# Performance work log

Hardware: AMD Instinct MI355X
Metric: run time of the kernel (lower is better)

The kernel has to match this reference:

```python
import jax, jax.numpy as jnp
import numpy as np

B, N, M, G = 2, 8192, 8192, 256
X_MIN = Y_MIN = -35.0
CELL = abs(2.0 * X_MIN / G)  # cell size, as in construct_batched_cuda_grid


def setup_inputs() -> dict:
    key = jax.random.key(0)
    k1, k2, k3, k4, k5 = jax.random.split(key, 5)
    p_i = jax.random.uniform(k1, (B, N, 3), jnp.float32, -34.0, 34.0)
    p_j = jax.random.uniform(k2, (B, M, 3), jnp.float32, -34.0, 34.0)
    mos = jax.random.normal(k3, (B, 2, G, G), jnp.float32)
    error_p_i_flow = jax.random.uniform(k4, (B, N), jnp.float32)
    nearest_flow = jax.random.randint(k5, (B, N, 1), 0, M, jnp.int32)
    return {"p_i": p_i, "mos": mos, "p_j": p_j,
            "error_p_i_flow": error_p_i_flow, "nearest_flow": nearest_flow}


def _knn1_l1(x, y):
    # brute-force 1-NN with L1 (norm=1) distance, matching knn_points(..., K=1, norm=1)
    # build (B,N,M) dist one coordinate at a time to avoid a (B,N,M,3) intermediate
    d = (jnp.abs(x[:, :, None, 0] - y[:, None, :, 0])
         + jnp.abs(x[:, :, None, 1] - y[:, None, :, 1])
         + jnp.abs(x[:, :, None, 2] - y[:, None, :, 2]))
    return jnp.min(d, axis=-1), jnp.argmin(d, axis=-1)


def reference(p_i, mos, p_j, error_p_i_flow, nearest_flow):
    # NN_loss with reduction='none' -> error_p_i_rigid = (cham_x + cham_y)/2 (needs N==M)
    cham_x, nearest_rigid = _knn1_l1(p_i, p_j)  # (B,N), (B,N)
    cham_y, _ = _knn1_l1(p_j, p_i)              # (B,M)
    error_p_i_rigid = (cham_x + cham_y) * 0.5

    dynamic = error_p_i_flow > error_p_i_rigid             # (B,N) bool
    idx = jnp.where(dynamic, nearest_flow[..., 0], nearest_rigid)  # (B,N)
    art_labels = dynamic.astype(jnp.int32)                 # (B,N) in {0,1}

    # batched gather p_j[b, idx[b]]
    p_j_by_nn = jnp.take_along_axis(p_j, idx[..., None], axis=1)  # (B,N,3)

    # construct_batched_cuda_grid: scatter labels into (B,G,G), -1 elsewhere
    shift = jnp.array([X_MIN, Y_MIN], jnp.float32)
    cell_idx = ((p_j_by_nn[:, :, :2] - shift) / CELL).astype(jnp.int32)  # (B,N,2)
    bs = jnp.repeat(jnp.arange(B), N)
    grid = -jnp.ones((B, G, G), jnp.int32)
    grid = grid.at[bs,
                   cell_idx[..., 0].reshape(-1),
                   cell_idx[..., 1].reshape(-1)].set(art_labels.reshape(-1))

    # CrossEntropyLoss(ignore_index=-1), mean over non-ignored cells
    logp = jax.nn.log_softmax(mos, axis=1)                 # (B,C,G,G)
    valid = grid >= 0
    tgt = jnp.clip(grid, 0, None)
    lp = jnp.take_along_axis(logp, tgt[:, None], axis=1)[:, 0]  # (B,G,G)
    loss = -jnp.where(valid, lp, 0.0).sum() / jnp.maximum(valid.sum(), 1).astype(lp.dtype)
    return loss
```

## Files before the change

### kernel.cpp

```cpp
#include <hip/hip_runtime.h>
#include <float.h>

#define B_ 2
#define N_ 8192
#define G_ 256
constexpr float X_MIN_F = -35.0f;
constexpr float CELL_F  = 0.2734375f;

using u64 = unsigned long long;

#define OFF_ACCUM 524288
#define OFF_PX    524352

template<int CC>
__global__ __launch_bounds__(256) void nn_kernel(const float* __restrict__ p_i,
                                                 const float* __restrict__ p_j,
                                                 u64* __restrict__ px,
                                                 float* __restrict__ py,
                                                 int* __restrict__ grid,
                                                 unsigned* __restrict__ accum)
{
    constexpr int COLS = N_ / CC;
    constexpr int NB   = 32 * CC;
    const int dir  = blockIdx.z >> 1;
    const int b    = blockIdx.z & 1;
    const int tid  = threadIdx.x;
    const int row0 = blockIdx.x * 1024 + tid * 4;
    const int c0   = blockIdx.y * COLS;

    const float* __restrict__ P = dir ? p_j : p_i;
    const float* __restrict__ Q = dir ? p_i : p_j;

    __shared__ __align__(16) float q[COLS * 3];
    for (int t = tid; t < COLS * 3 / 4; t += 256)
        ((float4*)q)[t] = ((const float4*)(Q + ((size_t)b * N_ + c0) * 3))[t];

    {
        const int lin = blockIdx.x + 8 * (blockIdx.y + CC * blockIdx.z);
        constexpr int PER = 32768 / NB;
        if (tid < PER)
            ((uint4*)grid)[lin * PER + tid] = make_uint4(~0u, ~0u, ~0u, ~0u);
        if (lin == 0 && tid < 4) accum[tid] = 0u;
    }

    const float4* pp = (const float4*)(P + ((size_t)b * N_ + row0) * 3);
    float4 r0 = pp[0], r1 = pp[1], r2 = pp[2];
    float px_[4] = {r0.x, r0.w, r1.z, r2.y};
    float py_[4] = {r0.y, r1.x, r1.w, r2.z};
    float pz_[4] = {r0.z, r1.y, r2.x, r2.w};

    float best[4];
#pragma unroll
    for (int r = 0; r < 4; r++) best[r] = FLT_MAX;

    __syncthreads();

    if (dir == 0) {
        int gcol[4] = {0, 0, 0, 0};
        for (int jg = 0; jg < COLS; jg += 8) {
            const float4* qv = (const float4*)&q[jg * 3];
            float4 v0 = qv[0], v1 = qv[1], v2 = qv[2];
            float4 v3 = qv[3], v4 = qv[4], v5 = qv[5];
            float qx[8] = {v0.x, v0.w, v1.z, v2.y, v3.x, v3.w, v4.z, v5.y};
            float qy[8] = {v0.y, v1.x, v1.w, v2.z, v3.y, v4.x, v4.w, v5.z};
            float qz[8] = {v0.z, v1.y, v2.x, v2.w, v3.z, v4.y, v5.x, v5.w};
#pragma unroll
            for (int r = 0; r < 4; r++) {
                float d[8];
#pragma unroll
                for (int k = 0; k < 8; k++)
                    d[k] = (fabsf(px_[r] - qx[k]) + fabsf(py_[r] - qy[k]))
                           + fabsf(pz_[r] - qz[k]);
                float m01 = fminf(d[0], d[1]), m23 = fminf(d[2], d[3]);
                float m45 = fminf(d[4], d[5]), m67 = fminf(d[6], d[7]);
                float m = fminf(fminf(m01, m23), fminf(m45, m67));
                bool lt = m < best[r];
                best[r] = lt ? m : best[r];
                gcol[r] = lt ? jg : gcol[r];
            }
        }
        int bidx[4];
#pragma unroll
        for (int r = 0; r < 4; r++) {
            const float4* qv = (const float4*)&q[gcol[r] * 3];
            float4 v0 = qv[0], v1 = qv[1], v2 = qv[2];
            float4 v3 = qv[3], v4 = qv[4], v5 = qv[5];
            float qx[8] = {v0.x, v0.w, v1.z, v2.y, v3.x, v3.w, v4.z, v5.y};
            float qy[8] = {v0.y, v1.x, v1.w, v2.z, v3.y, v4.x, v4.w, v5.z};
            float qz[8] = {v0.z, v1.y, v2.x, v2.w, v3.z, v4.y, v5.x, v5.w};
            int kk = 0;
#pragma unroll
            for (int k = 7; k >= 0; k--) {
                float d = (fabsf(px_[r] - qx[k]) + fabsf(py_[r] - qy[k]))
                          + fabsf(pz_[r] - qz[k]);
                kk = (d == best[r]) ? k : kk;
            }
            bidx[r] = c0 + gcol[r] + kk;
        }
        const size_t o = (size_t)blockIdx.y * (B_ * N_) + b * N_ + row0;
#pragma unroll
        for (int r = 0; r < 4; r++)
            px[o + r] = ((u64)__float_as_uint(best[r]) << 32) | (unsigned)bidx[r];
    } else {
        for (int jg = 0; jg < COLS; jg += 8) {
            const float4* qv = (const float4*)&q[jg * 3];
            float4 v0 = qv[0], v1 = qv[1], v2 = qv[2];
            float4 v3 = qv[3], v4 = qv[4], v5 = qv[5];
            float qx[8] = {v0.x, v0.w, v1.z, v2.y, v3.x, v3.w, v4.z, v5.y};
            float qy[8] = {v0.y, v1.x, v1.w, v2.z, v3.y, v4.x, v4.w, v5.z};
            float qz[8] = {v0.z, v1.y, v2.x, v2.w, v3.z, v4.y, v5.x, v5.w};
#pragma unroll
            for (int r = 0; r < 4; r++) {
#pragma unroll
                for (int k = 0; k < 8; k++) {
                    float d = (fabsf(px_[r] - qx[k]) + fabsf(py_[r] - qy[k]))
                              + fabsf(pz_[r] - qz[k]);
                    best[r] = fminf(best[r], d);
                }
            }
        }
        const size_t o = (size_t)blockIdx.y * (B_ * N_) + b * N_ + row0;
#pragma unroll
        for (int r = 0; r < 4; r++) py[o + r] = best[r];
    }
}

template<int CC>
__global__ __launch_bounds__(256) void reduce_scatter_kernel(
    const u64* __restrict__ px, const float* __restrict__ py,
    const float* __restrict__ flow, const int* __restrict__ nflow,
    const float* __restrict__ Pj, int* __restrict__ grid)
{
    __shared__ u64      sbx[64];
    __shared__ unsigned sby[64];
    const int tid = threadIdx.x;
    const int p   = tid & 63;
    const int g   = tid >> 6;
    constexpr int CPG = CC / 4;

    if (tid < 64) { sbx[tid] = ~0ull; sby[tid] = ~0u; }
    __syncthreads();

    const int pt = blockIdx.x * 64 + p;
    u64   bx = ~0ull;
    float by = FLT_MAX;
#pragma unroll
    for (int k = 0; k < CPG; k++) {
        int c = g * CPG + k;
        u64 v = px[(size_t)c * (B_ * N_) + pt];
        bx = v < bx ? v : bx;
        by = fminf(by, py[(size_t)c * (B_ * N_) + pt]);
    }
    atomicMin(&sbx[p], bx);
    atomicMin(&sby[p], __float_as_uint(by));
    __syncthreads();

    if (tid < 64) {
        u64 fx = sbx[tid];
        float dx = __uint_as_float((unsigned)(fx >> 32));
        float dy = __uint_as_float(sby[tid]);
        float rigid = (dx + dy) * 0.5f;

        const int i = blockIdx.x * 64 + tid;
        const int b = i >> 13;
        const int n = i & (N_ - 1);

        bool dyn  = flow[i] > rigid;
        int label = dyn ? 1 : 0;
        int idx   = dyn ? nflow[i] : (int)(unsigned)(fx & 0xFFFFFFFFull);

        const float* qp = Pj + ((size_t)b * N_ + idx) * 3;
        float xx = qp[0], yy = qp[1];

        int cx = (int)((xx - X_MIN_F) / CELL_F);
        int cy = (int)((yy - X_MIN_F) / CELL_F);

        atomicMax(&grid[(b << 16) + cx * G_ + cy], (n << 1) | label);
    }
}

__global__ __launch_bounds__(256) void ce_kernel(const float* __restrict__ mos,
                                                 const int* __restrict__ grid,
                                                 float* __restrict__ accum,
                                                 float* __restrict__ out)
{
    int i = blockIdx.x * 256 + threadIdx.x;
    float lsum = 0.0f;
    int   lcnt = 0;

    int packed = grid[i];
    if (packed >= 0) {
        int b    = i >> 16;
        int cell = i & 0xFFFF;
        float m0 = mos[((size_t)b * 2 + 0) * 65536 + cell];
        float m1 = mos[((size_t)b * 2 + 1) * 65536 + cell];
        float mx = fmaxf(m0, m1);
        float lse = logf(expf(m0 - mx) + expf(m1 - mx));
        float sh  = ((packed & 1) ? m1 : m0) - mx;
        lsum = sh - lse;
        lcnt = 1;
    }

#pragma unroll
    for (int o = 32; o > 0; o >>= 1) {
        lsum += __shfl_down(lsum, o);
        lcnt += __shfl_down(lcnt, o);
    }
    __shared__ float wsum[4];
    __shared__ int   wcnt[4];
    int wave = threadIdx.x >> 6;
    if ((threadIdx.x & 63) == 0) { wsum[wave] = lsum; wcnt[wave] = lcnt; }
    __syncthreads();
    if (threadIdx.x == 0) {
        float s = wsum[0] + wsum[1] + wsum[2] + wsum[3];
        int   c = wcnt[0] + wcnt[1] + wcnt[2] + wcnt[3];
        atomicAdd(&accum[0], s);
        atomicAdd((int*)&accum[1], c);
        __threadfence();
        unsigned t = atomicAdd((unsigned*)&accum[2], 1u);
        if (t == gridDim.x - 1) {
            float S = atomicAdd(&accum[0], 0.0f);
            int   C = atomicAdd((int*)&accum[1], 0);
            out[0] = -S / (float)(C > 0 ? C : 1);
        }
    }
}

template<int CC>
static void run(const float* p_i, const float* mos, const float* p_j,
                const float* flow, const int* nflow, float* out,
                char* ws, hipStream_t stream)
{
    int*   grid  = (int*)ws;
    float* accum = (float*)(ws + OFF_ACCUM);
    u64*   px    = (u64*)(ws + OFF_PX);
    float* py    = (float*)(ws + OFF_PX + (size_t)CC * B_ * N_ * 8);

    dim3 g(8, CC, 4);
    nn_kernel<CC><<<g, 256, 0, stream>>>(p_i, p_j, px, py, (int*)grid,
                                         (unsigned*)accum);
    reduce_scatter_kernel<CC><<<256, 256, 0, stream>>>(px, py, flow, nflow,
                                                       p_j, grid);
    ce_kernel<<<(B_ * G_ * G_) / 256, 256, 0, stream>>>(mos, grid, accum, out);
}

extern "C" void kernel_launch(void* const* d_in, const int* in_sizes, int n_in,
                              void* d_out, int out_size, void* d_ws, size_t ws_size,
                              hipStream_t stream)
{
    const float* p_i   = (const float*)d_in[0];
    const float* mos   = (const float*)d_in[1];
    const float* p_j   = (const float*)d_in[2];
    const float* flow  = (const float*)d_in[3];
    const int*   nflow = (const int*)d_in[4];
    float* out = (float*)d_out;
    char* ws = (char*)d_ws;

    if (ws_size >= OFF_PX + (size_t)64 * B_ * N_ * 12)
        run<64>(p_i, mos, p_j, flow, nflow, out, ws, stream);
    else if (ws_size >= OFF_PX + (size_t)32 * B_ * N_ * 12)
        run<32>(p_i, mos, p_j, flow, nflow, out, ws, stream);
    else
        run<8>(p_i, mos, p_j, flow, nflow, out, ws, stream);
}
```

Measured before the change: 128.1 us.

## Fuse both NN directions into one pass using symmetric distance column minima

The L1 distance is symmetric, so the second nearest-neighbour direction (p_j to p_i) no longer launches its own set of blocks. Instead, the p_i-row pass also reduces each distance tile along columns, using permlane32_swap, a per-wave LDS scratch and xor shuffles. Per-block column partial minima go to the workspace, and the reduce kernel merges the 8 row-block partials. This removes about half of the distance arithmetic and halves the grid, at the cost of extra cross-lane reduction work and LDS traffic in every 8-column step. The main loop now reads the query points from global memory, which are uniform per block, instead of from LDS.

```diff
diff --git a/kernel.cpp b/kernel.cpp
--- a/kernel.cpp
+++ b/kernel.cpp
@@ -16,24 +16,27 @@
 __global__ __launch_bounds__(256) void nn_kernel(const float* __restrict__ p_i,
                                                  const float* __restrict__ p_j,
                                                  u64* __restrict__ px,
-                                                 float* __restrict__ py,
+                                                 float* __restrict__ colpart,
                                                  int* __restrict__ grid,
                                                  unsigned* __restrict__ accum)
 {
     constexpr int COLS = N_ / CC;
-    constexpr int NB   = 32 * CC;
-    const int dir  = blockIdx.z >> 1;
-    const int b    = blockIdx.z & 1;
+    constexpr int NB   = 16 * CC;
+    const int b    = blockIdx.z;
     const int tid  = threadIdx.x;
+    const int lane = tid & 63;
+    const int w    = tid >> 6;
     const int row0 = blockIdx.x * 1024 + tid * 4;
     const int c0   = blockIdx.y * COLS;
 
-    const float* __restrict__ P = dir ? p_j : p_i;
-    const float* __restrict__ Q = dir ? p_i : p_j;
-
     __shared__ __align__(16) float q[COLS * 3];
+    __shared__ float sc[4][8][35];
+    __shared__ float colW[4][COLS];
+
+    const float* __restrict__ Qg = p_j + ((size_t)b * N_ + c0) * 3;
+
     for (int t = tid; t < COLS * 3 / 4; t += 256)
-        ((float4*)q)[t] = ((const float4*)(Q + ((size_t)b * N_ + c0) * 3))[t];
+        ((float4*)q)[t] = ((const float4*)Qg)[t];
 
     {
         const int lin = blockIdx.x + 8 * (blockIdx.y + CC * blockIdx.z);
@@ -43,91 +46,98 @@
         if (lin == 0 && tid < 4) accum[tid] = 0u;
     }
 
-    const float4* pp = (const float4*)(P + ((size_t)b * N_ + row0) * 3);
+    const float4* pp = (const float4*)(p_i + ((size_t)b * N_ + row0) * 3);
     float4 r0 = pp[0], r1 = pp[1], r2 = pp[2];
     float px_[4] = {r0.x, r0.w, r1.z, r2.y};
     float py_[4] = {r0.y, r1.x, r1.w, r2.z};
     float pz_[4] = {r0.z, r1.y, r2.x, r2.w};
 
-    float best[4];
-#pragma unroll
-    for (int r = 0; r < 4; r++) best[r] = FLT_MAX;
-
-    __syncthreads();
-
-    if (dir == 0) {
-        int gcol[4] = {0, 0, 0, 0};
-        for (int jg = 0; jg < COLS; jg += 8) {
-            const float4* qv = (const float4*)&q[jg * 3];
-            float4 v0 = qv[0], v1 = qv[1], v2 = qv[2];
-            float4 v3 = qv[3], v4 = qv[4], v5 = qv[5];
-            float qx[8] = {v0.x, v0.w, v1.z, v2.y, v3.x, v3.w, v4.z, v5.y};
-            float qy[8] = {v0.y, v1.x, v1.w, v2.z, v3.y, v4.x, v4.w, v5.z};
-            float qz[8] = {v0.z, v1.y, v2.x, v2.w, v3.z, v4.y, v5.x, v5.w};
-#pragma unroll
-            for (int r = 0; r < 4; r++) {
-                float d[8];
-#pragma unroll
-                for (int k = 0; k < 8; k++)
-                    d[k] = (fabsf(px_[r] - qx[k]) + fabsf(py_[r] - qy[k]))
+    float best[4] = {FLT_MAX, FLT_MAX, FLT_MAX, FLT_MAX};
+    int   gcol[4] = {0, 0, 0, 0};
+
+    for (int jg = 0; jg < COLS; jg += 8) {
+        const float4* qv = (const float4*)(Qg + (size_t)jg * 3);
+        float4 v0 = qv[0], v1 = qv[1], v2 = qv[2];
+        float4 v3 = qv[3], v4 = qv[4], v5 = qv[5];
+        float qx[8] = {v0.x, v0.w, v1.z, v2.y, v3.x, v3.w, v4.z, v5.y};
+        float qy[8] = {v0.y, v1.x, v1.w, v2.z, v3.y, v4.x, v4.w, v5.z};
+        float qz[8] = {v0.z, v1.y, v2.x, v2.w, v3.z, v4.y, v5.x, v5.w};
+
+        float dm[4][8];
+#pragma unroll
+        for (int r = 0; r < 4; r++) {
+#pragma unroll
+            for (int k = 0; k < 8; k++)
+                dm[r][k] = (fabsf(px_[r] - qx[k]) + fabsf(py_[r] - qy[k]))
                            + fabsf(pz_[r] - qz[k]);
-                float m01 = fminf(d[0], d[1]), m23 = fminf(d[2], d[3]);
-                float m45 = fminf(d[4], d[5]), m67 = fminf(d[6], d[7]);
-                float m = fminf(fminf(m01, m23), fminf(m45, m67));
-                bool lt = m < best[r];
-                best[r] = lt ? m : best[r];
-                gcol[r] = lt ? jg : gcol[r];
-            }
-        }
-        int bidx[4];
-#pragma unroll
-        for (int r = 0; r < 4; r++) {
-            const float4* qv = (const float4*)&q[gcol[r] * 3];
-            float4 v0 = qv[0], v1 = qv[1], v2 = qv[2];
-            float4 v3 = qv[3], v4 = qv[4], v5 = qv[5];
-            float qx[8] = {v0.x, v0.w, v1.z, v2.y, v3.x, v3.w, v4.z, v5.y};
-            float qy[8] = {v0.y, v1.x, v1.w, v2.z, v3.y, v4.x, v4.w, v5.z};
-            float qz[8] = {v0.z, v1.y, v2.x, v2.w, v3.z, v4.y, v5.x, v5.w};
-            int kk = 0;
-#pragma unroll
-            for (int k = 7; k >= 0; k--) {
-                float d = (fabsf(px_[r] - qx[k]) + fabsf(py_[r] - qy[k]))
-                          + fabsf(pz_[r] - qz[k]);
-                kk = (d == best[r]) ? k : kk;
-            }
-            bidx[r] = c0 + gcol[r] + kk;
-        }
-        const size_t o = (size_t)blockIdx.y * (B_ * N_) + b * N_ + row0;
-#pragma unroll
-        for (int r = 0; r < 4; r++)
-            px[o + r] = ((u64)__float_as_uint(best[r]) << 32) | (unsigned)bidx[r];
-    } else {
-        for (int jg = 0; jg < COLS; jg += 8) {
-            const float4* qv = (const float4*)&q[jg * 3];
-            float4 v0 = qv[0], v1 = qv[1], v2 = qv[2];
-            float4 v3 = qv[3], v4 = qv[4], v5 = qv[5];
-            float qx[8] = {v0.x, v0.w, v1.z, v2.y, v3.x, v3.w, v4.z, v5.y};
-            float qy[8] = {v0.y, v1.x, v1.w, v2.z, v3.y, v4.x, v4.w, v5.z};
-            float qz[8] = {v0.z, v1.y, v2.x, v2.w, v3.z, v4.y, v5.x, v5.w};
-#pragma unroll
-            for (int r = 0; r < 4; r++) {
-#pragma unroll
-                for (int k = 0; k < 8; k++) {
-                    float d = (fabsf(px_[r] - qx[k]) + fabsf(py_[r] - qy[k]))
-                              + fabsf(pz_[r] - qz[k]);
-                    best[r] = fminf(best[r], d);
-                }
-            }
-        }
-        const size_t o = (size_t)blockIdx.y * (B_ * N_) + b * N_ + row0;
-#pragma unroll
-        for (int r = 0; r < 4; r++) py[o + r] = best[r];
-    }
+            float m = fminf(fminf(dm[r][0], dm[r][1]), dm[r][2]);
+            m = fminf(fminf(m, dm[r][3]), dm[r][4]);
+            m = fminf(fminf(m, dm[r][5]), dm[r][6]);
+            m = fminf(m, dm[r][7]);
+            bool lt = m < best[r];
+            best[r] = lt ? m : best[r];
+            gcol[r] = lt ? jg : gcol[r];
+        }
+
+        float part[8];
+#pragma unroll
+        for (int k = 0; k < 8; k++)
+            part[k] = fminf(fminf(fminf(dm[0][k], dm[1][k]), dm[2][k]),
+                            dm[3][k]);
+
+#pragma unroll
+        for (int k = 0; k < 8; k++) {
+            unsigned a = __float_as_uint(part[k]);
+            auto pr = __builtin_amdgcn_permlane32_swap(a, a, false, false);
+            part[k] = fminf(__uint_as_float(pr[0]), __uint_as_float(pr[1]));
+        }
+#pragma unroll
+        for (int k = 0; k < 8; k++)
+            sc[w][k][lane & 31] = part[k];
+        const int kc = lane >> 3, mc = lane & 7;
+        float c4 = fminf(fminf(sc[w][kc][4 * mc],     sc[w][kc][4 * mc + 1]),
+                         fminf(sc[w][kc][4 * mc + 2], sc[w][kc][4 * mc + 3]));
+        c4 = fminf(c4, __shfl_xor(c4, 1));
+        c4 = fminf(c4, __shfl_xor(c4, 2));
+        c4 = fminf(c4, __shfl_xor(c4, 4));
+        if (mc == 0) colW[w][jg + kc] = c4;
+    }
+
+    __syncthreads();
+
+    for (int t = tid; t < COLS; t += 256) {
+        float c = fminf(fminf(colW[0][t], colW[1][t]),
+                        fminf(colW[2][t], colW[3][t]));
+        colpart[(size_t)blockIdx.x * (B_ * N_) + (size_t)b * N_ + c0 + t] = c;
+    }
+
+    int bidx[4];
+#pragma unroll
+    for (int r = 0; r < 4; r++) {
+        const float4* qv = (const float4*)&q[gcol[r] * 3];
+        float4 v0 = qv[0], v1 = qv[1], v2 = qv[2];
+        float4 v3 = qv[3], v4 = qv[4], v5 = qv[5];
+        float qx[8] = {v0.x, v0.w, v1.z, v2.y, v3.x, v3.w, v4.z, v5.y};
+        float qy[8] = {v0.y, v1.x, v1.w, v2.z, v3.y, v4.x, v4.w, v5.z};
+        float qz[8] = {v0.z, v1.y, v2.x, v2.w, v3.z, v4.y, v5.x, v5.w};
+        int kk = 0;
+#pragma unroll
+        for (int k = 7; k >= 0; k--) {
+            float d = (fabsf(px_[r] - qx[k]) + fabsf(py_[r] - qy[k]))
+                      + fabsf(pz_[r] - qz[k]);
+            kk = (d == best[r]) ? k : kk;
+        }
+        bidx[r] = c0 + gcol[r] + kk;
+    }
+    const size_t o = (size_t)blockIdx.y * (B_ * N_) + b * N_ + row0;
+#pragma unroll
+    for (int r = 0; r < 4; r++)
+        px[o + r] = ((u64)__float_as_uint(best[r]) << 32) | (unsigned)bidx[r];
 }
 
 template<int CC>
 __global__ __launch_bounds__(256) void reduce_scatter_kernel(
-    const u64* __restrict__ px, const float* __restrict__ py,
+    const u64* __restrict__ px, const float* __restrict__ cp,
     const float* __restrict__ flow, const int* __restrict__ nflow,
     const float* __restrict__ Pj, int* __restrict__ grid)
 {
@@ -142,15 +152,15 @@
     __syncthreads();
 
     const int pt = blockIdx.x * 64 + p;
-    u64   bx = ~0ull;
-    float by = FLT_MAX;
+    u64 bx = ~0ull;
 #pragma unroll
     for (int k = 0; k < CPG; k++) {
         int c = g * CPG + k;
         u64 v = px[(size_t)c * (B_ * N_) + pt];
         bx = v < bx ? v : bx;
-        by = fminf(by, py[(size_t)c * (B_ * N_) + pt]);
-    }
+    }
+    float by = fminf(cp[(size_t)(2 * g)     * (B_ * N_) + pt],
+                     cp[(size_t)(2 * g + 1) * (B_ * N_) + pt]);
     atomicMin(&sbx[p], bx);
     atomicMin(&sby[p], __float_as_uint(by));
     __syncthreads();
@@ -231,16 +241,16 @@
                 const float* flow, const int* nflow, float* out,
                 char* ws, hipStream_t stream)
 {
-    int*   grid  = (int*)ws;
-    float* accum = (float*)(ws + OFF_ACCUM);
-    u64*   px    = (u64*)(ws + OFF_PX);
-    float* py    = (float*)(ws + OFF_PX + (size_t)CC * B_ * N_ * 8);
-
-    dim3 g(8, CC, 4);
-    nn_kernel<CC><<<g, 256, 0, stream>>>(p_i, p_j, px, py, (int*)grid,
+    int*   grid    = (int*)ws;
+    float* accum   = (float*)(ws + OFF_ACCUM);
+    u64*   px      = (u64*)(ws + OFF_PX);
+    float* colpart = (float*)(ws + OFF_PX + (size_t)CC * B_ * N_ * 8);
+
+    dim3 g(8, CC, 2);
+    nn_kernel<CC><<<g, 256, 0, stream>>>(p_i, p_j, px, colpart, (int*)grid,
                                          (unsigned*)accum);
-    reduce_scatter_kernel<CC><<<256, 256, 0, stream>>>(px, py, flow, nflow,
-                                                       p_j, grid);
+    reduce_scatter_kernel<CC><<<256, 256, 0, stream>>>(px, colpart, flow,
+                                                       nflow, p_j, grid);
     ce_kernel<<<(B_ * G_ * G_) / 256, 256, 0, stream>>>(mos, grid, accum, out);
 }
 
@@ -256,9 +266,10 @@
     float* out = (float*)d_out;
     char* ws = (char*)d_ws;
 
-    if (ws_size >= OFF_PX + (size_t)64 * B_ * N_ * 12)
+    constexpr size_t CPART = (size_t)8 * B_ * N_ * 4;
+    if (ws_size >= OFF_PX + (size_t)64 * B_ * N_ * 8 + CPART)
         run<64>(p_i, mos, p_j, flow, nflow, out, ws, stream);
-    else if (ws_size >= OFF_PX + (size_t)32 * B_ * N_ * 12)
+    else if (ws_size >= OFF_PX + (size_t)32 * B_ * N_ * 8 + CPART)
         run<32>(p_i, mos, p_j, flow, nflow, out, ws, stream);
     else
         run<8>(p_i, mos, p_j, flow, nflow, out, ws, stream);
```

After: 116.8 us. -8.8%, faster.
